# Performance work log

Measured on AMD Instinct MI355X. Metric: run time of the kernel, lower is better.

Reference implementation:

```python
import jax, jax.numpy as jnp
import numpy as np

N_NODES = 50000
N_EDGES = 800000
NODE_IN = 256
EDGE_OUT = 64
GLOBAL_IN = 128
NODE_OUT = 256
HIDDEN = 512
N_GRAPHS = 64


def setup_inputs() -> dict:
    key = jax.random.key(0)
    ks = jax.random.split(key, 8)
    x = jax.random.normal(ks[0], (N_NODES, NODE_IN), dtype=jnp.float32)
    edge_index = jax.random.randint(ks[1], (2, N_EDGES), 0, N_NODES, dtype=jnp.int64)
    edge_attr = jax.random.normal(ks[2], (N_EDGES, EDGE_OUT), dtype=jnp.float32)
    u = jax.random.normal(ks[3], (N_GRAPHS, GLOBAL_IN), dtype=jnp.float32)
    batch = jnp.sort(jax.random.randint(ks[4], (N_NODES,), 0, N_GRAPHS, dtype=jnp.int64))
    in_dim = NODE_IN + EDGE_OUT + GLOBAL_IN
    # MLP params (torch nn.Linear default init: U(-1/sqrt(fan_in), 1/sqrt(fan_in)))
    b1s = 1.0 / np.sqrt(in_dim)
    b2s = 1.0 / np.sqrt(HIDDEN)
    W1 = jax.random.uniform(ks[5], (in_dim, HIDDEN), dtype=jnp.float32, minval=-b1s, maxval=b1s)
    b1 = jnp.zeros((HIDDEN,), dtype=jnp.float32)
    W2 = jax.random.uniform(ks[6], (HIDDEN, NODE_OUT), dtype=jnp.float32, minval=-b2s, maxval=b2s)
    b2 = jnp.zeros((NODE_OUT,), dtype=jnp.float32)
    return {"x": x, "edge_index": edge_index, "edge_attr": edge_attr, "u": u,
            "batch": batch, "W1": W1, "b1": b1, "W2": W2, "b2": b2}


def reference(x, edge_index, edge_attr, u, batch, W1, b1, W2, b2):
    n = x.shape[0]
    src = edge_index[0]
    # scatter_mean(edge_attr, src, dim=0, dim_size=n)
    sums = jax.ops.segment_sum(edge_attr, src, num_segments=n)          # [N, E_out]
    counts = jax.ops.segment_sum(jnp.ones((edge_attr.shape[0],), edge_attr.dtype),
                                 src, num_segments=n)                   # [N]
    edge_attr_agg = sums / jnp.maximum(counts, 1.0)[:, None]
    u_expanded = u[batch]                                               # [N, G_in]
    combined = jnp.concatenate([x, edge_attr_agg, u_expanded], axis=1)  # [N, 448]
    h = jax.nn.relu(combined @ W1 + b1)                                 # [N, H]
    return h @ W2 + b2                                                  # [N, N_out]
```

## Files before the change

kernel.cpp:

```cpp
#include <hip/hip_runtime.h>
#include <hip/hip_bf16.h>
#include <stdint.h>

#define NN 50000
#define NE 800000
#define NODE_IN 256
#define EDGE_OUT 64
#define GLOBAL_IN 128
#define NODE_OUT 256
#define HIDDEN 512
#define K1 320
#define N_GRAPHS 64
#define MAXDEG 64

typedef __attribute__((ext_vector_type(8))) short bf16x8;
typedef __attribute__((ext_vector_type(4))) float f32x4;
typedef __attribute__((ext_vector_type(4))) unsigned short us4;

__device__ __forceinline__ unsigned short f2bf(float x) {
    union { float f; unsigned int u; } c; c.f = x;
    unsigned int u = c.u;
    unsigned int r = (u + 0x7FFFu + ((u >> 16) & 1u)) >> 16;
    return (unsigned short)r;
}

#define GLD_LDS(gp, lp) __builtin_amdgcn_global_load_lds( \
    (const __attribute__((address_space(1))) unsigned int*)(gp), \
    (__attribute__((address_space(3))) unsigned int*)(lp), 16, 0, 0)

#define PREP_W1 (HIDDEN * K1)
#define PREP_W2 (PREP_W1 + NODE_OUT * HIDDEN)
#define PREP_G  (PREP_W2 + N_GRAPHS * HIDDEN)
#define PREP_Z  (PREP_G + NN)
__global__ __launch_bounds__(256)
void prep(const float* __restrict__ W1, const float* __restrict__ W2,
          const float* __restrict__ u, const float* __restrict__ b1,
          unsigned short* __restrict__ W1T, unsigned short* __restrict__ W2T,
          float* __restrict__ G, int* __restrict__ cnt)
{
    int idx = blockIdx.x * 256 + threadIdx.x;
    if (idx < PREP_W1) {
        int n = idx / K1, k = idx - n * K1;
        W1T[idx] = f2bf(W1[(size_t)k * HIDDEN + n]);
    } else if (idx < PREP_W2) {
        int j = idx - PREP_W1;
        int n = j / HIDDEN, k = j - n * HIDDEN;
        W2T[j] = f2bf(W2[(size_t)k * NODE_OUT + n]);
    } else if (idx < PREP_G) {
        int j = idx - PREP_W2;
        int g = j >> 9, col = j & 511;
        const float* up = u + (size_t)g * GLOBAL_IN;
        float acc = b1[col];
        #pragma unroll 4
        for (int k = 0; k < GLOBAL_IN; ++k)
            acc += up[k] * W1[(size_t)(K1 + k) * HIDDEN + col];
        G[j] = acc;
    } else if (idx < PREP_Z) {
        cnt[idx - PREP_G] = 0;
    }
}

__global__ __launch_bounds__(256)
void fill_perm(const int* __restrict__ src, int* __restrict__ cnt,
               int* __restrict__ perm)
{
    int e = blockIdx.x * 256 + threadIdx.x;
    if (e < NE) {
        int s = src[e];
        int pos = atomicAdd(&cnt[s], 1);
        if (pos < MAXDEG) perm[(size_t)s * MAXDEG + pos] = e;
    }
}

__global__ __launch_bounds__(256)
void seg_comb(const float* __restrict__ edge_attr,
              const int* __restrict__ perm,
              const int* __restrict__ cnt,
              const float* __restrict__ x,
              unsigned short* __restrict__ comb)
{
    int node = blockIdx.x * 4 + (threadIdx.x >> 6);
    if (node >= NN) return;
    int lane = threadIdx.x & 63;
    unsigned short* crow = comb + (size_t)node * K1;

    {
        const float4 v = *(const float4*)(x + (size_t)node * NODE_IN + lane * 4);
        us4 o = { f2bf(v.x), f2bf(v.y), f2bf(v.z), f2bf(v.w) };
        *(us4*)(crow + lane * 4) = o;
    }
    int c = cnt[node];
    int cc = c < MAXDEG ? c : MAXDEG;
    int g = lane >> 4;
    int f = (lane & 15) * 4;
    const int* pbase = perm + (size_t)node * MAXDEG;
    float4 a0 = make_float4(0.f, 0.f, 0.f, 0.f);
    float4 a1 = make_float4(0.f, 0.f, 0.f, 0.f);
    int i = g;
    for (; i + 4 < cc; i += 8) {
        int e0 = pbase[i];
        int e1 = pbase[i + 4];
        const float4 v0 = *(const float4*)(edge_attr + (size_t)e0 * EDGE_OUT + f);
        const float4 v1 = *(const float4*)(edge_attr + (size_t)e1 * EDGE_OUT + f);
        a0.x += v0.x; a0.y += v0.y; a0.z += v0.z; a0.w += v0.w;
        a1.x += v1.x; a1.y += v1.y; a1.z += v1.z; a1.w += v1.w;
    }
    if (i < cc) {
        int e0 = pbase[i];
        const float4 v0 = *(const float4*)(edge_attr + (size_t)e0 * EDGE_OUT + f);
        a0.x += v0.x; a0.y += v0.y; a0.z += v0.z; a0.w += v0.w;
    }
    float4 acc = make_float4(a0.x + a1.x, a0.y + a1.y, a0.z + a1.z, a0.w + a1.w);
    #pragma unroll
    for (int off = 16; off < 64; off <<= 1) {
        acc.x += __shfl_xor(acc.x, off, 64);
        acc.y += __shfl_xor(acc.y, off, 64);
        acc.z += __shfl_xor(acc.z, off, 64);
        acc.w += __shfl_xor(acc.w, off, 64);
    }
    if (g == 0) {
        float inv = 1.0f / fmaxf((float)c, 1.0f);
        us4 o = { f2bf(acc.x * inv), f2bf(acc.y * inv),
                  f2bf(acc.z * inv), f2bf(acc.w * inv) };
        *(us4*)(crow + NODE_IN + f) = o;
    }
}

template<int EPI>
__global__ __launch_bounds__(256)
void gemm_bt_128(const unsigned short* __restrict__ A,
                 const unsigned short* __restrict__ B,
                 const float* __restrict__ bias,
                 const int* __restrict__ batch,
                 void* __restrict__ Cv,
                 int M, int N, int K)
{
    __shared__ unsigned short lA[128 * 64];
    __shared__ unsigned short lB[128 * 64];
    const int tid = threadIdx.x;
    const int w = tid >> 6, l = tid & 63;

    const int nwg  = gridDim.x * gridDim.y;
    const int orig = blockIdx.x + gridDim.x * blockIdx.y;
    const int q = nwg >> 3, r = nwg & 7;
    const int xcd = orig & 7, sidx = orig >> 3;
    const int wg = (xcd < r ? xcd * (q + 1) : r * (q + 1) + (xcd - r) * q) + sidx;
    const int m0 = (wg / gridDim.x) * 128;
    const int n0 = (wg % gridDim.x) * 128;

    const int wr = w >> 1, wc = w & 1;

    f32x4 acc[4][4] = {};

    const unsigned short* pAs[4];
    const unsigned short* pBs[4];
    #pragma unroll
    for (int i = 0; i < 4; ++i) {
        int c = tid + i * 256;
        int row = c >> 3;
        int kg = ((c & 7) ^ (row & 7)) * 8;
        int gr = m0 + row; if (gr >= M) gr = M - 1;
        pAs[i] = A + (size_t)gr * K + kg;
        pBs[i] = B + (size_t)(n0 + row) * K + kg;
    }

    for (int k0 = 0; k0 < K; k0 += 64) {
        #pragma unroll
        for (int i = 0; i < 4; ++i)
            GLD_LDS(pAs[i] + k0, &lA[(size_t)(tid + i * 256) * 8]);
        #pragma unroll
        for (int i = 0; i < 4; ++i)
            GLD_LDS(pBs[i] + k0, &lB[(size_t)(tid + i * 256) * 8]);
        __syncthreads();

        #pragma unroll
        for (int kk = 0; kk < 2; ++kk) {
            bf16x8 af[4], bfr[4];
            #pragma unroll
            for (int m = 0; m < 4; ++m) {
                int ar = wr * 64 + m * 16 + (l & 15);
                int gran = (kk * 4 + (l >> 4)) ^ (ar & 7);
                af[m] = *(const bf16x8*)&lA[ar * 64 + gran * 8];
            }
            #pragma unroll
            for (int n = 0; n < 4; ++n) {
                int br = wc * 64 + n * 16 + (l & 15);
                int gran = (kk * 4 + (l >> 4)) ^ (br & 7);
                bfr[n] = *(const bf16x8*)&lB[br * 64 + gran * 8];
            }
            #pragma unroll
            for (int m = 0; m < 4; ++m)
                #pragma unroll
                for (int n = 0; n < 4; ++n)
                    acc[m][n] = __builtin_amdgcn_mfma_f32_16x16x32_bf16(af[m], bfr[n], acc[m][n], 0, 0, 0);
        }
        __syncthreads();
    }

    const int cbase = n0 + wc * 64 + (l & 15);
    const int rbase = m0 + wr * 64 + ((l >> 4) << 2);
    if (EPI == 0) {
        unsigned short* C = (unsigned short*)Cv;
        #pragma unroll
        for (int m = 0; m < 4; ++m) {
            #pragma unroll
            for (int j = 0; j < 4; ++j) {
                int row = rbase + m * 16 + j;
                if (row < M) {
                    const float* grow = bias + (size_t)batch[row] * HIDDEN;
                    #pragma unroll
                    for (int n = 0; n < 4; ++n) {
                        int c = cbase + n * 16;
                        float v = acc[m][n][j] + grow[c];
                        v = fmaxf(v, 0.0f);
                        C[(size_t)row * N + c] = f2bf(v);
                    }
                }
            }
        }
    } else {
        float* C = (float*)Cv;
        #pragma unroll
        for (int m = 0; m < 4; ++m) {
            #pragma unroll
            for (int j = 0; j < 4; ++j) {
                int row = rbase + m * 16 + j;
                if (row < M) {
                    #pragma unroll
                    for (int n = 0; n < 4; ++n) {
                        int c = cbase + n * 16;
                        C[(size_t)row * N + c] = acc[m][n][j] + bias[c];
                    }
                }
            }
        }
    }
}

extern "C" void kernel_launch(void* const* d_in, const int* in_sizes, int n_in,
                              void* d_out, int out_size, void* d_ws, size_t ws_size,
                              hipStream_t stream)
{
    const float* x         = (const float*)d_in[0];
    const int*   edge_idx  = (const int*)d_in[1];
    const float* edge_attr = (const float*)d_in[2];
    const float* u         = (const float*)d_in[3];
    const int*   batch     = (const int*)d_in[4];
    const float* W1        = (const float*)d_in[5];
    const float* b1        = (const float*)d_in[6];
    const float* W2        = (const float*)d_in[7];
    const float* b2        = (const float*)d_in[8];
    float* out = (float*)d_out;

    char* ws = (char*)d_ws;
    int*            cnt    = (int*)(ws);
    int*            perm   = (int*)(ws + 200704);
    unsigned short* comb   = (unsigned short*)(ws + 13000704);
    unsigned short* W1T    = (unsigned short*)(ws + 45000704);
    unsigned short* W2T    = (unsigned short*)(ws + 45328384);
    float*          G      = (float*)(ws + 45590528);
    unsigned short* h      = (unsigned short*)(ws + 45721600);

    prep<<<(PREP_Z + 255) / 256, 256, 0, stream>>>(W1, W2, u, b1, W1T, W2T, G, cnt);

    fill_perm<<<(NE + 255) / 256, 256, 0, stream>>>(edge_idx, cnt, perm);

    seg_comb<<<(NN + 3) / 4, 256, 0, stream>>>(edge_attr, perm, cnt, x, comb);

    gemm_bt_128<0><<<dim3(HIDDEN / 128, (NN + 127) / 128), 256, 0, stream>>>(
        comb, W1T, G, batch, h, NN, HIDDEN, K1);
    gemm_bt_128<1><<<dim3(NODE_OUT / 128, (NN + 127) / 128), 256, 0, stream>>>(
        h, W2T, b2, nullptr, out, NN, NODE_OUT, HIDDEN);
}
```

Before: 213.3 us.

## Move x-to-bf16 copy into the perm-fill kernel and shuffle-broadcast perm indices

The x-row bf16 conversion moves out of the segment-mean kernel into the atomic perm-fill kernel, which now runs as a grid-stride loop over 2048 blocks. The intent is to overlap streaming x conversion with the latency-bound atomic scatter. The segment kernel now loads each node's perm row once per lane and broadcasts edge ids with shuffles, replacing repeated scalar index loads. The tradeoff is that the fill kernel does more serial work per thread, and the perm load reads all 64 slots even when degree is small.

```diff
diff --git a/kernel.cpp b/kernel.cpp
--- a/kernel.cpp
+++ b/kernel.cpp
@@ -61,54 +61,52 @@
 }
 
 __global__ __launch_bounds__(256)
-void fill_perm(const int* __restrict__ src, int* __restrict__ cnt,
-               int* __restrict__ perm)
-{
-    int e = blockIdx.x * 256 + threadIdx.x;
-    if (e < NE) {
+void fillx(const int* __restrict__ src, int* __restrict__ cnt,
+           int* __restrict__ perm, const float* __restrict__ x,
+           unsigned short* __restrict__ comb)
+{
+    const int gs = gridDim.x * 256;
+    for (int e = blockIdx.x * 256 + threadIdx.x; e < NE; e += gs) {
         int s = src[e];
         int pos = atomicAdd(&cnt[s], 1);
         if (pos < MAXDEG) perm[(size_t)s * MAXDEG + pos] = e;
     }
-}
-
-__global__ __launch_bounds__(256)
-void seg_comb(const float* __restrict__ edge_attr,
-              const int* __restrict__ perm,
-              const int* __restrict__ cnt,
-              const float* __restrict__ x,
-              unsigned short* __restrict__ comb)
+    for (int q = blockIdx.x * 256 + threadIdx.x; q < NN * 64; q += gs) {
+        int node = q >> 6, lane = q & 63;
+        const float4 v = *(const float4*)(x + (size_t)node * NODE_IN + lane * 4);
+        us4 o = { f2bf(v.x), f2bf(v.y), f2bf(v.z), f2bf(v.w) };
+        *(us4*)(comb + (size_t)node * K1 + lane * 4) = o;
+    }
+}
+
+__global__ __launch_bounds__(256)
+void seg(const float* __restrict__ edge_attr, const int* __restrict__ perm,
+         const int* __restrict__ cnt, unsigned short* __restrict__ comb)
 {
     int node = blockIdx.x * 4 + (threadIdx.x >> 6);
     if (node >= NN) return;
     int lane = threadIdx.x & 63;
-    unsigned short* crow = comb + (size_t)node * K1;
-
-    {
-        const float4 v = *(const float4*)(x + (size_t)node * NODE_IN + lane * 4);
-        us4 o = { f2bf(v.x), f2bf(v.y), f2bf(v.z), f2bf(v.w) };
-        *(us4*)(crow + lane * 4) = o;
-    }
+    int g = lane >> 4, f = (lane & 15) * 4;
     int c = cnt[node];
     int cc = c < MAXDEG ? c : MAXDEG;
-    int g = lane >> 4;
-    int f = (lane & 15) * 4;
     const int* pbase = perm + (size_t)node * MAXDEG;
+    int eperm = pbase[lane];
     float4 a0 = make_float4(0.f, 0.f, 0.f, 0.f);
     float4 a1 = make_float4(0.f, 0.f, 0.f, 0.f);
-    int i = g;
-    for (; i + 4 < cc; i += 8) {
-        int e0 = pbase[i];
-        int e1 = pbase[i + 4];
-        const float4 v0 = *(const float4*)(edge_attr + (size_t)e0 * EDGE_OUT + f);
-        const float4 v1 = *(const float4*)(edge_attr + (size_t)e1 * EDGE_OUT + f);
-        a0.x += v0.x; a0.y += v0.y; a0.z += v0.z; a0.w += v0.w;
-        a1.x += v1.x; a1.y += v1.y; a1.z += v1.z; a1.w += v1.w;
-    }
-    if (i < cc) {
-        int e0 = pbase[i];
-        const float4 v0 = *(const float4*)(edge_attr + (size_t)e0 * EDGE_OUT + f);
-        a0.x += v0.x; a0.y += v0.y; a0.z += v0.z; a0.w += v0.w;
+    const int nb = (cc + 7) >> 3;
+    for (int kb = 0; kb < nb; ++kb) {
+        int i0 = (kb << 3) + g;
+        int i1 = i0 + 4;
+        int e0 = __shfl(eperm, i0, 64);
+        int e1 = __shfl(eperm, i1, 64);
+        if (i0 < cc) {
+            const float4 v0 = *(const float4*)(edge_attr + (size_t)e0 * EDGE_OUT + f);
+            a0.x += v0.x; a0.y += v0.y; a0.z += v0.z; a0.w += v0.w;
+        }
+        if (i1 < cc) {
+            const float4 v1 = *(const float4*)(edge_attr + (size_t)e1 * EDGE_OUT + f);
+            a1.x += v1.x; a1.y += v1.y; a1.z += v1.z; a1.w += v1.w;
+        }
     }
     float4 acc = make_float4(a0.x + a1.x, a0.y + a1.y, a0.z + a1.z, a0.w + a1.w);
     #pragma unroll
@@ -122,7 +120,7 @@
         float inv = 1.0f / fmaxf((float)c, 1.0f);
         us4 o = { f2bf(acc.x * inv), f2bf(acc.y * inv),
                   f2bf(acc.z * inv), f2bf(acc.w * inv) };
-        *(us4*)(crow + NODE_IN + f) = o;
+        *(us4*)(comb + (size_t)node * K1 + NODE_IN + f) = o;
     }
 }
 
@@ -242,7 +240,7 @@
                               hipStream_t stream)
 {
     const float* x         = (const float*)d_in[0];
-    const int*   edge_idx  = (const int*)d_in[1];
+    const int*   src       = (const int*)d_in[1];
     const float* edge_attr = (const float*)d_in[2];
     const float* u         = (const float*)d_in[3];
     const int*   batch     = (const int*)d_in[4];
@@ -263,9 +261,9 @@
 
     prep<<<(PREP_Z + 255) / 256, 256, 0, stream>>>(W1, W2, u, b1, W1T, W2T, G, cnt);
 
-    fill_perm<<<(NE + 255) / 256, 256, 0, stream>>>(edge_idx, cnt, perm);
-
-    seg_comb<<<(NN + 3) / 4, 256, 0, stream>>>(edge_attr, perm, cnt, x, comb);
+    fillx<<<2048, 256, 0, stream>>>(src, cnt, perm, x, comb);
+
+    seg<<<(NN + 3) / 4, 256, 0, stream>>>(edge_attr, perm, cnt, comb);
 
     gemm_bt_128<0><<<dim3(HIDDEN / 128, (NN + 127) / 128), 256, 0, stream>>>(
         comb, W1T, G, batch, h, NN, HIDDEN, K1);
```

After: 206.4 us. 1.03x faster.
